# Optimization experiments

Hardware: AMD Instinct MI355X
Metric: run time of the kernel (lower is better)

The kernel has to match this reference:

```python
import jax, jax.numpy as jnp
import numpy as np

TEMPERATURE = 0.5
LAMBDA_REG = 0.1
NUM_GROUPS = 4  # number of distinct sensitive-attribute values
EPS = 1e-8      # torch cosine_similarity norm clamp


def setup_inputs() -> dict:
    key = jax.random.key(0)
    k1, k2, k3 = jax.random.split(key, 3)
    B, D = 4096, 256
    return {
        "z_i": jax.random.normal(k1, (B, D), dtype=jnp.float32),
        "z_j": jax.random.normal(k2, (B, D), dtype=jnp.float32),
        "sensitive_features": jax.random.randint(k3, (B,), 0, NUM_GROUPS, dtype=jnp.int64),
    }


def reference(z_i, z_j, sensitive_features):
    B = z_i.shape[0]
    z = jnp.concatenate([z_i, z_j], axis=0)                       # [2B, D]
    norm = jnp.maximum(jnp.linalg.norm(z, axis=1, keepdims=True), EPS)
    zn = z / norm                                                  # row-normalized
    S = zn @ zn.T                                                  # [2B, 2B] cosine sims

    # NT-Xent contrastive term
    pos = jnp.concatenate([jnp.diagonal(S, offset=B), jnp.diagonal(S, offset=-B)])  # [2B]
    mask = 1.0 - jnp.eye(2 * B, dtype=S.dtype)                     # zero out self-sims
    den = jnp.sum(mask * jnp.exp(S / TEMPERATURE), axis=1)         # [2B]
    contrastive = jnp.sum(-(pos / TEMPERATURE) + jnp.log(den)) / (2 * B)

    # Fairness penalty over groups of the FIRST B rows (indices come from sensitive_features)
    Sg = S[:B, :B]
    onehot = jax.nn.one_hot(sensitive_features, NUM_GROUPS, dtype=S.dtype)  # [B, G]
    group_sums = jnp.sum(onehot * (Sg @ onehot), axis=0)           # [G] sum_{i,j in g} S[i,j] (incl. diag, as torch)
    counts = jnp.sum(onehot, axis=0)                               # [G]
    per_group = jnp.where(counts > 1, group_sums / (counts * (counts - 1.0)), 0.0)
    num_unique = jnp.sum(counts > 0).astype(S.dtype)
    fairness = LAMBDA_REG * (jnp.sum(per_group) / num_unique)

    return contrastive + fairness
```

## Files before the change

kernel.cpp:

```cpp
#include <hip/hip_runtime.h>
#include <hip/hip_bf16.h>

typedef __attribute__((ext_vector_type(8))) short short8;
typedef __attribute__((ext_vector_type(4))) float f32x4;
typedef __attribute__((address_space(1))) const void gvoid_t;
typedef __attribute__((address_space(3))) void lvoid_t;

#define NB 4096
#define DD 256
#define TWOB 8192
#define NMACRO 1056u
#define GSUM_BLOCKS 16
#define NPART 1072u

__device__ __forceinline__ unsigned short f2bf(float f) {
  unsigned int u = __float_as_uint(f);
  u += 0x7fffu + ((u >> 16) & 1u);
  return (unsigned short)(u >> 16);
}
__device__ __forceinline__ float bf2f(unsigned short s) {
  return __uint_as_float(((unsigned int)s) << 16);
}


__global__ __launch_bounds__(256) void norm_kernel(const float* __restrict__ zi,
                                                   const float* __restrict__ zj,
                                                   float* __restrict__ wsf,
                                                   float* __restrict__ ppos,
                                                   unsigned short* __restrict__ znb) {
  __shared__ float sred[4];
  if (blockIdx.x < 32) wsf[blockIdx.x * 256 + threadIdx.x] = 0.f;
  const int lane = threadIdx.x & 63, wave = threadIdx.x >> 6;
  const int i = blockIdx.x * 4 + wave;

  float4 a = ((const float4*)(zi + (size_t)i * DD))[lane];
  float4 b = ((const float4*)(zj + (size_t)i * DD))[lane];
  float sa = a.x * a.x + a.y * a.y + a.z * a.z + a.w * a.w;
  float sb = b.x * b.x + b.y * b.y + b.z * b.z + b.w * b.w;
  float sab = a.x * b.x + a.y * b.y + a.z * b.z + a.w * b.w;
#pragma unroll
  for (int m = 32; m >= 1; m >>= 1) {
    sa += __shfl_xor(sa, m);
    sb += __shfl_xor(sb, m);
    sab += __shfl_xor(sab, m);
  }
  float ra = 1.0f / fmaxf(sqrtf(sa), 1e-8f);
  float rb = 1.0f / fmaxf(sqrtf(sb), 1e-8f);
  ushort4 oa, ob;
  oa.x = f2bf(a.x * ra); oa.y = f2bf(a.y * ra); oa.z = f2bf(a.z * ra); oa.w = f2bf(a.w * ra);
  ob.x = f2bf(b.x * rb); ob.y = f2bf(b.y * rb); ob.z = f2bf(b.z * rb); ob.w = f2bf(b.w * rb);
  ((ushort4*)(znb + (size_t)i * DD))[lane] = oa;
  ((ushort4*)(znb + (size_t)(i + NB) * DD))[lane] = ob;

  if (lane == 0) sred[wave] = sab * ra * rb;
  __syncthreads();
  if (threadIdx.x == 0)
    ppos[blockIdx.x] = sred[0] + sred[1] + sred[2] + sred[3];
}

__global__ __launch_bounds__(512, 4) void den_kernel(const int* __restrict__ sf,
                                                     float* __restrict__ wsf,
                                                     const unsigned short* __restrict__ znb,
                                                     float* __restrict__ vsum_part,
                                                     int* __restrict__ cnt_part) {
  __shared__ __align__(16) unsigned short As[3][4096];
  __shared__ __align__(16) unsigned short Bs[3][8192];

  float* den = wsf;

  const int tid = threadIdx.x;
  const int lane = tid & 63, wave = tid >> 6;
  const unsigned t_raw = blockIdx.y * 64u + blockIdx.x;
  if (t_raw >= NPART) return;
  const unsigned t_lin = (t_raw & 7u) * 134u + (t_raw >> 3);

  if (t_lin < GSUM_BLOCKS) {
    const int b = (int)t_lin;
    const int r0 = b * 256;
    float acc[4][4];
#pragma unroll
    for (int q = 0; q < 4; ++q)
#pragma unroll
      for (int e = 0; e < 4; ++e) acc[q][e] = 0.f;
    int cnt[4] = {0, 0, 0, 0};
    const int rw = r0 + wave * 32;
    for (int k = 0; k < 32; ++k) {
      int row = rw + k;
      int g = sf[row];
      ushort4 v = ((const ushort4*)(znb + (size_t)row * DD))[lane];
      float f0 = bf2f(v.x), f1 = bf2f(v.y), f2 = bf2f(v.z), f3 = bf2f(v.w);
#pragma unroll
      for (int q = 0; q < 4; ++q) {
        bool sel = (g == q);
        acc[q][0] += sel ? f0 : 0.f;
        acc[q][1] += sel ? f1 : 0.f;
        acc[q][2] += sel ? f2 : 0.f;
        acc[q][3] += sel ? f3 : 0.f;
        cnt[q] += sel ? 1 : 0;
      }
    }
    float4* lsd = (float4*)&Bs[0][0];
    int* lcnt = (int*)&As[0][0];
#pragma unroll
    for (int q = 0; q < 4; ++q) {
      float4 t;
      t.x = acc[q][0]; t.y = acc[q][1]; t.z = acc[q][2]; t.w = acc[q][3];
      lsd[(wave * 4 + q) * 64 + lane] = t;
    }
    if (lane == 0) {
#pragma unroll
      for (int q = 0; q < 4; ++q) lcnt[wave * 4 + q] = cnt[q];
    }
    __syncthreads();
    if (tid < 256) {
      int g = tid >> 6, l = tid & 63;
      float4 s = {0.f, 0.f, 0.f, 0.f};
#pragma unroll
      for (int w = 0; w < 8; ++w) {
        float4 sv = lsd[(w * 4 + g) * 64 + l];
        s.x += sv.x; s.y += sv.y; s.z += sv.z; s.w += sv.w;
      }
      ((float4*)(vsum_part + (size_t)(b * 4 + g) * 256))[l] = s;
      if (tid < 4) {
        int ci = 0;
#pragma unroll
        for (int w = 0; w < 8; ++w) ci += lcnt[w * 4 + tid];
        cnt_part[b * 4 + tid] = ci;
      }
    }
    return;
  }

  unsigned t = t_lin - GSUM_BLOCKS;
  unsigned tr = 0;
  while (t >= 32u - (tr >> 1)) { t -= 32u - (tr >> 1); ++tr; }
  unsigned c = (tr >> 1) + t;
  const size_t rowbase = (size_t)tr * 128;
  const size_t colbase = (size_t)c * 256;

  const int u = lane >> 3;
  const int cp = (lane & 7) ^ u;
  const int ri = 2 * u + (cp >> 2);
  const int kelem = (cp & 3) * 8;
  const int slot = ((((lane & 1) << 2) | (lane >> 4)) ^ ((lane >> 1) & 7));
  const int fragoff = ((lane & 15) >> 1) * 128 + slot * 16;
  const int wrow = wave & 1;
  const int wcol = wave >> 1;

  const int tch = (int)(2 * c) + (wcol >> 1);
  const float fr = (tch >= (int)tr) ? 1.f : 0.f;
  const float fc = (tch > (int)tr) ? 1.f : 0.f;

  f32x4 zero = {0.f, 0.f, 0.f, 0.f};
  f32x4 acc[4][4];
#pragma unroll
  for (int i = 0; i < 4; ++i)
#pragma unroll
    for (int j = 0; j < 4; ++j) acc[i][j] = zero;

  const unsigned short* gA = znb + (rowbase + wave * 16 + ri) * DD + kelem;
  const unsigned short* gB0 = znb + (colbase + (2 * wave) * 16 + ri) * DD + kelem;
  const unsigned short* gB1 = gB0 + 16 * DD;

  auto stage = [&](int kt, int buf) {
    __builtin_amdgcn_global_load_lds((gvoid_t*)(gA + kt * 32), (lvoid_t*)&As[buf][wave * 512], 16, 0, 0);
    __builtin_amdgcn_global_load_lds((gvoid_t*)(gB0 + kt * 32), (lvoid_t*)&Bs[buf][(2 * wave) * 512], 16, 0, 0);
    __builtin_amdgcn_global_load_lds((gvoid_t*)(gB1 + kt * 32), (lvoid_t*)&Bs[buf][(2 * wave + 1) * 512], 16, 0, 0);
  };

  stage(0, 0);
  stage(1, 1);
#pragma unroll
  for (int kt = 0; kt < 8; ++kt) {
    const int buf = kt % 3;
    if (kt < 7) asm volatile("s_waitcnt vmcnt(3)" ::: "memory");
    else        asm volatile("s_waitcnt vmcnt(0)" ::: "memory");
    __builtin_amdgcn_s_barrier();
    asm volatile("" ::: "memory");
    if (kt < 6) stage(kt + 2, (kt + 2) % 3);
    short8 af[4], bfr[4];
#pragma unroll
    for (int mi = 0; mi < 4; ++mi)
      af[mi] = *(const short8*)((const char*)&As[0][0] + buf * 8192 + (wrow * 4 + mi) * 1024 + fragoff);
#pragma unroll
    for (int ni = 0; ni < 4; ++ni)
      bfr[ni] = *(const short8*)((const char*)&Bs[0][0] + buf * 16384 + (wcol * 4 + ni) * 1024 + fragoff);
#pragma unroll
    for (int mi = 0; mi < 4; ++mi)
#pragma unroll
      for (int ni = 0; ni < 4; ++ni)
        acc[mi][ni] = __builtin_amdgcn_mfma_f32_16x16x32_bf16(af[mi], bfr[ni], acc[mi][ni], 0, 0, 0);
  }

  float rsum[4][4];
  float csum[4];
#pragma unroll
  for (int mi = 0; mi < 4; ++mi)
#pragma unroll
    for (int r = 0; r < 4; ++r) rsum[mi][r] = 0.f;
#pragma unroll
  for (int ni = 0; ni < 4; ++ni) csum[ni] = 0.f;
#pragma unroll
  for (int mi = 0; mi < 4; ++mi)
#pragma unroll
    for (int ni = 0; ni < 4; ++ni)
#pragma unroll
      for (int r = 0; r < 4; ++r) {
        float e = __expf(2.0f * acc[mi][ni][r]);
        rsum[mi][r] += e;
        csum[ni] += e;
      }
#pragma unroll
  for (int m = 1; m < 16; m <<= 1)
#pragma unroll
    for (int mi = 0; mi < 4; ++mi)
#pragma unroll
      for (int r = 0; r < 4; ++r) rsum[mi][r] += __shfl_xor(rsum[mi][r], m);
#pragma unroll
  for (int m = 16; m < 64; m <<= 1)
#pragma unroll
    for (int ni = 0; ni < 4; ++ni) csum[ni] += __shfl_xor(csum[ni], m);

  float* Lr = (float*)&As[0][0];
  float* Lc = Lr + 512;
  if ((lane & 15) == 0) {
    int h = lane >> 4;
#pragma unroll
    for (int mi = 0; mi < 4; ++mi)
#pragma unroll
      for (int r = 0; r < 4; ++r)
        Lr[wcol * 128 + wrow * 64 + mi * 16 + h * 4 + r] = rsum[mi][r] * fr;
  }
  if (lane < 16) {
#pragma unroll
    for (int ni = 0; ni < 4; ++ni)
      Lc[wrow * 256 + wcol * 64 + ni * 16 + lane] = csum[ni] * fc;
  }
  __syncthreads();
  if (tid < 256) {
    float v = Lc[tid] + Lc[256 + tid];
    if (v != 0.f) unsafeAtomicAdd(&den[colbase + tid], v);
  } else if (tid < 384) {
    int r = tid - 256;
    unsafeAtomicAdd(&den[rowbase + r], Lr[r] + Lr[128 + r] + Lr[256 + r] + Lr[384 + r]);
  }
}

__global__ __launch_bounds__(1024) void tail_kernel(const float* __restrict__ wsf,
                                                    const float* __restrict__ vsum_part,
                                                    const int* __restrict__ cnt_part,
                                                    const float* __restrict__ ppos,
                                                    float* __restrict__ out) {
  __shared__ float sred[48];
  const float* den = wsf;
  const int tid = threadIdx.x;
  const int lane = tid & 63, wave = tid >> 6;

  const float e2 = __expf(2.0f);
  float ls = 0.f;
#pragma unroll
  for (int k = 0; k < 8; ++k) ls += __logf(den[k * 1024 + tid] - e2);
#pragma unroll
  for (int m = 32; m >= 1; m >>= 1) ls += __shfl_xor(ls, m);
  if (lane == 0) sred[wave] = ls;

  float pp = ppos[tid];
#pragma unroll
  for (int m = 32; m >= 1; m >>= 1) pp += __shfl_xor(pp, m);
  if (lane == 0) sred[16 + wave] = pp;

  {
    int g = tid >> 8, col = tid & 255;
    float v = 0.f;
#pragma unroll
    for (int b = 0; b < 16; ++b) v += vsum_part[(size_t)(b * 4 + g) * 256 + col];
    float gp = v * v;
#pragma unroll
    for (int m = 32; m >= 1; m >>= 1) gp += __shfl_xor(gp, m);
    if (lane == 0) sred[32 + wave] = gp;
  }
  __syncthreads();
  if (tid == 0) {
    float lsum = 0.f, psum = 0.f;
#pragma unroll
    for (int w = 0; w < 16; ++w) { lsum += sred[w]; psum += sred[16 + w]; }
    float contrastive = (lsum - 4.0f * psum) / (float)TWOB;
    float fsum = 0.f;
    int uniq = 0;
#pragma unroll
    for (int q = 0; q < 4; ++q) {
      int ci = 0;
#pragma unroll
      for (int b = 0; b < 16; ++b) ci += cnt_part[b * 4 + q];
      float gsq = sred[32 + q * 4] + sred[33 + q * 4] + sred[34 + q * 4] + sred[35 + q * 4];
      float cf = (float)ci;
      if (ci > 0) uniq++;
      if (ci > 1) fsum += gsq / (cf * (cf - 1.0f));
    }
    out[0] = contrastive + 0.1f * (fsum / (uniq > 0 ? (float)uniq : 1.0f));
  }
}

extern "C" void kernel_launch(void* const* d_in, const int* in_sizes, int n_in,
                              void* d_out, int out_size, void* d_ws, size_t ws_size,
                              hipStream_t stream) {
  const float* zi = (const float*)d_in[0];
  const float* zj = (const float*)d_in[1];
  const int* sf = (const int*)d_in[2];
  float* out = (float*)d_out;
  char* ws = (char*)d_ws;
  float* wsf = (float*)ws;
  unsigned short* znb = (unsigned short*)(ws + 65536);
  float* vsum_part = (float*)(ws + 4259840);
  int* cnt_part = (int*)(ws + 4276224);
  float* ppos = (float*)(ws + 4276480);

  hipLaunchKernelGGL(norm_kernel, dim3(1024), dim3(256), 0, stream, zi, zj, wsf, ppos, znb);
  hipLaunchKernelGGL(den_kernel, dim3(64, 17), dim3(512), 0, stream,
                     sf, wsf, znb, vsum_part, cnt_part);
  hipLaunchKernelGGL(tail_kernel, dim3(1), dim3(1024), 0, stream,
                     wsf, vsum_part, cnt_part, ppos, out);
}
```

Baseline: 96.65 us.

## Use 256x256 symmetric tiles in den_kernel instead of 128x256

Result: slower. 102.0 us (+5.5%).

```diff
diff --git a/kernel.cpp b/kernel.cpp
--- a/kernel.cpp
+++ b/kernel.cpp
@@ -9,9 +9,9 @@
 #define NB 4096
 #define DD 256
 #define TWOB 8192
-#define NMACRO 1056u
+#define NMACRO 528u
 #define GSUM_BLOCKS 16
-#define NPART 1072u
+#define NPART 544u
 
 __device__ __forceinline__ unsigned short f2bf(float f) {
   unsigned int u = __float_as_uint(f);
@@ -58,21 +58,21 @@
     ppos[blockIdx.x] = sred[0] + sred[1] + sred[2] + sred[3];
 }
 
-__global__ __launch_bounds__(512, 4) void den_kernel(const int* __restrict__ sf,
+__global__ __launch_bounds__(512, 2) void den_kernel(const int* __restrict__ sf,
                                                      float* __restrict__ wsf,
                                                      const unsigned short* __restrict__ znb,
                                                      float* __restrict__ vsum_part,
                                                      int* __restrict__ cnt_part) {
-  __shared__ __align__(16) unsigned short As[3][4096];
+  __shared__ __align__(16) unsigned short As[3][8192];
   __shared__ __align__(16) unsigned short Bs[3][8192];
 
   float* den = wsf;
 
   const int tid = threadIdx.x;
   const int lane = tid & 63, wave = tid >> 6;
-  const unsigned t_raw = blockIdx.y * 64u + blockIdx.x;
+  const unsigned t_raw = blockIdx.y * 68u + blockIdx.x;
   if (t_raw >= NPART) return;
-  const unsigned t_lin = (t_raw & 7u) * 134u + (t_raw >> 3);
+  const unsigned t_lin = (t_raw & 7u) * 68u + (t_raw >> 3);
 
   if (t_lin < GSUM_BLOCKS) {
     const int b = (int)t_lin;
@@ -133,10 +133,11 @@
 
   unsigned t = t_lin - GSUM_BLOCKS;
   unsigned tr = 0;
-  while (t >= 32u - (tr >> 1)) { t -= 32u - (tr >> 1); ++tr; }
-  unsigned c = (tr >> 1) + t;
-  const size_t rowbase = (size_t)tr * 128;
-  const size_t colbase = (size_t)c * 256;
+  while (t >= 32u - tr) { t -= 32u - tr; ++tr; }
+  unsigned tc = tr + t;
+  const size_t rowbase = (size_t)tr * 256;
+  const size_t colbase = (size_t)tc * 256;
+  const bool offdiag = (tc > tr);
 
   const int u = lane >> 3;
   const int cp = (lane & 7) ^ u;
@@ -144,26 +145,24 @@
   const int kelem = (cp & 3) * 8;
   const int slot = ((((lane & 1) << 2) | (lane >> 4)) ^ ((lane >> 1) & 7));
   const int fragoff = ((lane & 15) >> 1) * 128 + slot * 16;
-  const int wrow = wave & 1;
-  const int wcol = wave >> 1;
-
-  const int tch = (int)(2 * c) + (wcol >> 1);
-  const float fr = (tch >= (int)tr) ? 1.f : 0.f;
-  const float fc = (tch > (int)tr) ? 1.f : 0.f;
+  const int wrow = wave >> 1;
+  const int wcol = wave & 1;
 
   f32x4 zero = {0.f, 0.f, 0.f, 0.f};
-  f32x4 acc[4][4];
+  f32x4 acc[4][8];
 #pragma unroll
   for (int i = 0; i < 4; ++i)
 #pragma unroll
-    for (int j = 0; j < 4; ++j) acc[i][j] = zero;
-
-  const unsigned short* gA = znb + (rowbase + wave * 16 + ri) * DD + kelem;
+    for (int j = 0; j < 8; ++j) acc[i][j] = zero;
+
+  const unsigned short* gA0 = znb + (rowbase + (2 * wave) * 16 + ri) * DD + kelem;
+  const unsigned short* gA1 = gA0 + 16 * DD;
   const unsigned short* gB0 = znb + (colbase + (2 * wave) * 16 + ri) * DD + kelem;
   const unsigned short* gB1 = gB0 + 16 * DD;
 
   auto stage = [&](int kt, int buf) {
-    __builtin_amdgcn_global_load_lds((gvoid_t*)(gA + kt * 32), (lvoid_t*)&As[buf][wave * 512], 16, 0, 0);
+    __builtin_amdgcn_global_load_lds((gvoid_t*)(gA0 + kt * 32), (lvoid_t*)&As[buf][(2 * wave) * 512], 16, 0, 0);
+    __builtin_amdgcn_global_load_lds((gvoid_t*)(gA1 + kt * 32), (lvoid_t*)&As[buf][(2 * wave + 1) * 512], 16, 0, 0);
     __builtin_amdgcn_global_load_lds((gvoid_t*)(gB0 + kt * 32), (lvoid_t*)&Bs[buf][(2 * wave) * 512], 16, 0, 0);
     __builtin_amdgcn_global_load_lds((gvoid_t*)(gB1 + kt * 32), (lvoid_t*)&Bs[buf][(2 * wave + 1) * 512], 16, 0, 0);
   };
@@ -173,37 +172,37 @@
 #pragma unroll
   for (int kt = 0; kt < 8; ++kt) {
     const int buf = kt % 3;
-    if (kt < 7) asm volatile("s_waitcnt vmcnt(3)" ::: "memory");
+    if (kt < 7) asm volatile("s_waitcnt vmcnt(4)" ::: "memory");
     else        asm volatile("s_waitcnt vmcnt(0)" ::: "memory");
     __builtin_amdgcn_s_barrier();
     asm volatile("" ::: "memory");
     if (kt < 6) stage(kt + 2, (kt + 2) % 3);
-    short8 af[4], bfr[4];
+    short8 af[4], bfr[8];
 #pragma unroll
     for (int mi = 0; mi < 4; ++mi)
-      af[mi] = *(const short8*)((const char*)&As[0][0] + buf * 8192 + (wrow * 4 + mi) * 1024 + fragoff);
-#pragma unroll
-    for (int ni = 0; ni < 4; ++ni)
-      bfr[ni] = *(const short8*)((const char*)&Bs[0][0] + buf * 16384 + (wcol * 4 + ni) * 1024 + fragoff);
+      af[mi] = *(const short8*)((const char*)&As[0][0] + buf * 16384 + (wrow * 4 + mi) * 1024 + fragoff);
+#pragma unroll
+    for (int ni = 0; ni < 8; ++ni)
+      bfr[ni] = *(const short8*)((const char*)&Bs[0][0] + buf * 16384 + (wcol * 8 + ni) * 1024 + fragoff);
 #pragma unroll
     for (int mi = 0; mi < 4; ++mi)
 #pragma unroll
-      for (int ni = 0; ni < 4; ++ni)
+      for (int ni = 0; ni < 8; ++ni)
         acc[mi][ni] = __builtin_amdgcn_mfma_f32_16x16x32_bf16(af[mi], bfr[ni], acc[mi][ni], 0, 0, 0);
   }
 
   float rsum[4][4];
-  float csum[4];
+  float csum[8];
 #pragma unroll
   for (int mi = 0; mi < 4; ++mi)
 #pragma unroll
     for (int r = 0; r < 4; ++r) rsum[mi][r] = 0.f;
 #pragma unroll
-  for (int ni = 0; ni < 4; ++ni) csum[ni] = 0.f;
+  for (int ni = 0; ni < 8; ++ni) csum[ni] = 0.f;
 #pragma unroll
   for (int mi = 0; mi < 4; ++mi)
 #pragma unroll
-    for (int ni = 0; ni < 4; ++ni)
+    for (int ni = 0; ni < 8; ++ni)
 #pragma unroll
       for (int r = 0; r < 4; ++r) {
         float e = __expf(2.0f * acc[mi][ni][r]);
@@ -219,7 +218,7 @@
 #pragma unroll
   for (int m = 16; m < 64; m <<= 1)
 #pragma unroll
-    for (int ni = 0; ni < 4; ++ni) csum[ni] += __shfl_xor(csum[ni], m);
+    for (int ni = 0; ni < 8; ++ni) csum[ni] += __shfl_xor(csum[ni], m);
 
   float* Lr = (float*)&As[0][0];
   float* Lc = Lr + 512;
@@ -229,20 +228,20 @@
     for (int mi = 0; mi < 4; ++mi)
 #pragma unroll
       for (int r = 0; r < 4; ++r)
-        Lr[wcol * 128 + wrow * 64 + mi * 16 + h * 4 + r] = rsum[mi][r] * fr;
+        Lr[wcol * 256 + wrow * 64 + mi * 16 + h * 4 + r] = rsum[mi][r];
   }
   if (lane < 16) {
 #pragma unroll
-    for (int ni = 0; ni < 4; ++ni)
-      Lc[wrow * 256 + wcol * 64 + ni * 16 + lane] = csum[ni] * fc;
+    for (int ni = 0; ni < 8; ++ni)
+      Lc[wrow * 256 + wcol * 128 + ni * 16 + lane] = csum[ni];
   }
   __syncthreads();
   if (tid < 256) {
-    float v = Lc[tid] + Lc[256 + tid];
-    if (v != 0.f) unsafeAtomicAdd(&den[colbase + tid], v);
-  } else if (tid < 384) {
-    int r = tid - 256;
-    unsafeAtomicAdd(&den[rowbase + r], Lr[r] + Lr[128 + r] + Lr[256 + r] + Lr[384 + r]);
+    unsafeAtomicAdd(&den[rowbase + tid], Lr[tid] + Lr[256 + tid]);
+  } else if (offdiag) {
+    int cc = tid - 256;
+    unsafeAtomicAdd(&den[colbase + cc],
+                    Lc[cc] + Lc[256 + cc] + Lc[512 + cc] + Lc[768 + cc]);
   }
 }
 
@@ -316,7 +315,7 @@
   float* ppos = (float*)(ws + 4276480);
 
   hipLaunchKernelGGL(norm_kernel, dim3(1024), dim3(256), 0, stream, zi, zj, wsf, ppos, znb);
-  hipLaunchKernelGGL(den_kernel, dim3(64, 17), dim3(512), 0, stream,
+  hipLaunchKernelGGL(den_kernel, dim3(68, 8), dim3(512), 0, stream,
                      sf, wsf, znb, vsum_part, cnt_part);
   hipLaunchKernelGGL(tail_kernel, dim3(1), dim3(1024), 0, stream,
                      wsf, vsum_part, cnt_part, ppos, out);
```

## Fuse tail reduction into den kernel and process two tiles per block

Applied to the files above, without the earlier changes.

Measured after the change: 106.5 us. 10.2% more time.

```diff
diff --git a/kernel.cpp b/kernel.cpp
--- a/kernel.cpp
+++ b/kernel.cpp
@@ -11,7 +11,7 @@
 #define TWOB 8192
 #define NMACRO 1056u
 #define GSUM_BLOCKS 16
-#define NPART 1072u
+#define NPART 544u
 
 __device__ __forceinline__ unsigned short f2bf(float f) {
   unsigned int u = __float_as_uint(f);
@@ -30,6 +30,7 @@
                                                    unsigned short* __restrict__ znb) {
   __shared__ float sred[4];
   if (blockIdx.x < 32) wsf[blockIdx.x * 256 + threadIdx.x] = 0.f;
+  if (blockIdx.x == 32 && threadIdx.x == 0) ((int*)(wsf + 8192))[0] = 0;
   const int lane = threadIdx.x & 63, wave = threadIdx.x >> 6;
   const int i = blockIdx.x * 4 + wave;
 
@@ -62,17 +63,20 @@
                                                      float* __restrict__ wsf,
                                                      const unsigned short* __restrict__ znb,
                                                      float* __restrict__ vsum_part,
-                                                     int* __restrict__ cnt_part) {
+                                                     int* __restrict__ cnt_part,
+                                                     const float* __restrict__ ppos,
+                                                     float* __restrict__ out,
+                                                     int* __restrict__ done_cnt) {
   __shared__ __align__(16) unsigned short As[3][4096];
   __shared__ __align__(16) unsigned short Bs[3][8192];
+  __shared__ __align__(16) float Escr[1024];
+  __shared__ int ilast;
 
   float* den = wsf;
-
   const int tid = threadIdx.x;
   const int lane = tid & 63, wave = tid >> 6;
-  const unsigned t_raw = blockIdx.y * 64u + blockIdx.x;
-  if (t_raw >= NPART) return;
-  const unsigned t_lin = (t_raw & 7u) * 134u + (t_raw >> 3);
+  const unsigned t_raw = blockIdx.y * 68u + blockIdx.x;
+  const unsigned t_lin = (t_raw & 7u) * 68u + (t_raw >> 3);
 
   if (t_lin < GSUM_BLOCKS) {
     const int b = (int)t_lin;
@@ -128,176 +132,206 @@
         cnt_part[b * 4 + tid] = ci;
       }
     }
-    return;
+  } else {
+    const unsigned idx = t_lin - GSUM_BLOCKS;
+    unsigned tr0, c0, tr1, c1;
+    {
+      unsigned t = 2u * idx, tr = 0;
+      while (t >= 32u - (tr >> 1)) { t -= 32u - (tr >> 1); ++tr; }
+      tr0 = tr; c0 = (tr >> 1) + t;
+      t = 2u * idx + 1u; tr = 0;
+      while (t >= 32u - (tr >> 1)) { t -= 32u - (tr >> 1); ++tr; }
+      tr1 = tr; c1 = (tr >> 1) + t;
+    }
+
+    const int u = lane >> 3;
+    const int cp = (lane & 7) ^ u;
+    const int ri = 2 * u + (cp >> 2);
+    const int kelem = (cp & 3) * 8;
+    const int slot = ((((lane & 1) << 2) | (lane >> 4)) ^ ((lane >> 1) & 7));
+    const int fragoff = ((lane & 15) >> 1) * 128 + slot * 16;
+    const int wrow = wave & 1;
+    const int wcol = wave >> 1;
+
+    f32x4 zero = {0.f, 0.f, 0.f, 0.f};
+    f32x4 acc[4][4];
+#pragma unroll
+    for (int i = 0; i < 4; ++i)
+#pragma unroll
+      for (int j = 0; j < 4; ++j) acc[i][j] = zero;
+
+    const unsigned short* gA_p0 = znb + ((size_t)tr0 * 128 + wave * 16 + ri) * DD + kelem;
+    const unsigned short* gB0_p0 = znb + ((size_t)c0 * 256 + (2 * wave) * 16 + ri) * DD + kelem;
+    const unsigned short* gB1_p0 = gB0_p0 + 16 * DD;
+    const unsigned short* gA_p1 = znb + ((size_t)tr1 * 128 + wave * 16 + ri) * DD + kelem;
+    const unsigned short* gB0_p1 = znb + ((size_t)c1 * 256 + (2 * wave) * 16 + ri) * DD + kelem;
+    const unsigned short* gB1_p1 = gB0_p1 + 16 * DD;
+
+    auto stage = [&](int s) {
+      const int buf = s % 3, kt = s & 7;
+      const unsigned short* gA = (s < 8) ? gA_p0 : gA_p1;
+      const unsigned short* gB0 = (s < 8) ? gB0_p0 : gB0_p1;
+      const unsigned short* gB1 = (s < 8) ? gB1_p0 : gB1_p1;
+      __builtin_amdgcn_global_load_lds((gvoid_t*)(gA + kt * 32), (lvoid_t*)&As[buf][wave * 512], 16, 0, 0);
+      __builtin_amdgcn_global_load_lds((gvoid_t*)(gB0 + kt * 32), (lvoid_t*)&Bs[buf][(2 * wave) * 512], 16, 0, 0);
+      __builtin_amdgcn_global_load_lds((gvoid_t*)(gB1 + kt * 32), (lvoid_t*)&Bs[buf][(2 * wave + 1) * 512], 16, 0, 0);
+    };
+
+    auto epilogue = [&](unsigned tr, unsigned c) {
+      const size_t rowbase = (size_t)tr * 128;
+      const size_t colbase = (size_t)c * 256;
+      const int tch = (int)(2 * c) + (wcol >> 1);
+      const float fr = (tch >= (int)tr) ? 1.f : 0.f;
+      const float fc = (tch > (int)tr) ? 1.f : 0.f;
+      float rsum[4][4], csum[4];
+#pragma unroll
+      for (int mi = 0; mi < 4; ++mi)
+#pragma unroll
+        for (int r = 0; r < 4; ++r) rsum[mi][r] = 0.f;
+#pragma unroll
+      for (int ni = 0; ni < 4; ++ni) csum[ni] = 0.f;
+#pragma unroll
+      for (int mi = 0; mi < 4; ++mi)
+#pragma unroll
+        for (int ni = 0; ni < 4; ++ni)
+#pragma unroll
+          for (int r = 0; r < 4; ++r) {
+            float e = __expf(2.0f * acc[mi][ni][r]);
+            rsum[mi][r] += e;
+            csum[ni] += e;
+          }
+#pragma unroll
+      for (int m = 1; m < 16; m <<= 1)
+#pragma unroll
+        for (int mi = 0; mi < 4; ++mi)
+#pragma unroll
+          for (int r = 0; r < 4; ++r) rsum[mi][r] += __shfl_xor(rsum[mi][r], m);
+#pragma unroll
+      for (int m = 16; m < 64; m <<= 1)
+#pragma unroll
+        for (int ni = 0; ni < 4; ++ni) csum[ni] += __shfl_xor(csum[ni], m);
+
+      float* Lr = &Escr[0];
+      float* Lc = &Escr[512];
+      if ((lane & 15) == 0) {
+        int h = lane >> 4;
+#pragma unroll
+        for (int mi = 0; mi < 4; ++mi)
+#pragma unroll
+          for (int r = 0; r < 4; ++r)
+            Lr[wcol * 128 + wrow * 64 + mi * 16 + h * 4 + r] = rsum[mi][r] * fr;
+      }
+      if (lane < 16) {
+#pragma unroll
+        for (int ni = 0; ni < 4; ++ni)
+          Lc[wrow * 256 + wcol * 64 + ni * 16 + lane] = csum[ni] * fc;
+      }
+      asm volatile("s_waitcnt lgkmcnt(0)" ::: "memory");
+      __builtin_amdgcn_s_barrier();
+      asm volatile("" ::: "memory");
+      if (tid < 256) {
+        float v = Lc[tid] + Lc[256 + tid];
+        if (v != 0.f) unsafeAtomicAdd(&den[colbase + tid], v);
+      } else if (tid < 384) {
+        int r = tid - 256;
+        unsafeAtomicAdd(&den[rowbase + r], Lr[r] + Lr[128 + r] + Lr[256 + r] + Lr[384 + r]);
+      }
+#pragma unroll
+      for (int i = 0; i < 4; ++i)
+#pragma unroll
+        for (int j = 0; j < 4; ++j) acc[i][j] = zero;
+    };
+
+    stage(0);
+    stage(1);
+#pragma unroll
+    for (int s = 0; s < 16; ++s) {
+      const int buf = s % 3;
+      if (s < 15) asm volatile("s_waitcnt vmcnt(4)" ::: "memory");
+      else        asm volatile("s_waitcnt vmcnt(0)" ::: "memory");
+      __builtin_amdgcn_s_barrier();
+      asm volatile("" ::: "memory");
+      if (s < 14) stage(s + 2);
+      short8 af[4], bfr[4];
+#pragma unroll
+      for (int mi = 0; mi < 4; ++mi)
+        af[mi] = *(const short8*)((const char*)&As[0][0] + buf * 8192 + (wrow * 4 + mi) * 1024 + fragoff);
+#pragma unroll
+      for (int ni = 0; ni < 4; ++ni)
+        bfr[ni] = *(const short8*)((const char*)&Bs[0][0] + buf * 16384 + (wcol * 4 + ni) * 1024 + fragoff);
+#pragma unroll
+      for (int mi = 0; mi < 4; ++mi)
+#pragma unroll
+        for (int ni = 0; ni < 4; ++ni)
+          acc[mi][ni] = __builtin_amdgcn_mfma_f32_16x16x32_bf16(af[mi], bfr[ni], acc[mi][ni], 0, 0, 0);
+      if (s == 7) epilogue(tr0, c0);
+    }
+    epilogue(tr1, c1);
   }
 
-  unsigned t = t_lin - GSUM_BLOCKS;
-  unsigned tr = 0;
-  while (t >= 32u - (tr >> 1)) { t -= 32u - (tr >> 1); ++tr; }
-  unsigned c = (tr >> 1) + t;
-  const size_t rowbase = (size_t)tr * 128;
-  const size_t colbase = (size_t)c * 256;
-
-  const int u = lane >> 3;
-  const int cp = (lane & 7) ^ u;
-  const int ri = 2 * u + (cp >> 2);
-  const int kelem = (cp & 3) * 8;
-  const int slot = ((((lane & 1) << 2) | (lane >> 4)) ^ ((lane >> 1) & 7));
-  const int fragoff = ((lane & 15) >> 1) * 128 + slot * 16;
-  const int wrow = wave & 1;
-  const int wcol = wave >> 1;
-
-  const int tch = (int)(2 * c) + (wcol >> 1);
-  const float fr = (tch >= (int)tr) ? 1.f : 0.f;
-  const float fc = (tch > (int)tr) ? 1.f : 0.f;
-
-  f32x4 zero = {0.f, 0.f, 0.f, 0.f};
-  f32x4 acc[4][4];
-#pragma unroll
-  for (int i = 0; i < 4; ++i)
-#pragma unroll
-    for (int j = 0; j < 4; ++j) acc[i][j] = zero;
-
-  const unsigned short* gA = znb + (rowbase + wave * 16 + ri) * DD + kelem;
-  const unsigned short* gB0 = znb + (colbase + (2 * wave) * 16 + ri) * DD + kelem;
-  const unsigned short* gB1 = gB0 + 16 * DD;
-
-  auto stage = [&](int kt, int buf) {
-    __builtin_amdgcn_global_load_lds((gvoid_t*)(gA + kt * 32), (lvoid_t*)&As[buf][wave * 512], 16, 0, 0);
-    __builtin_amdgcn_global_load_lds((gvoid_t*)(gB0 + kt * 32), (lvoid_t*)&Bs[buf][(2 * wave) * 512], 16, 0, 0);
-    __builtin_amdgcn_global_load_lds((gvoid_t*)(gB1 + kt * 32), (lvoid_t*)&Bs[buf][(2 * wave + 1) * 512], 16, 0, 0);
-  };
-
-  stage(0, 0);
-  stage(1, 1);
-#pragma unroll
-  for (int kt = 0; kt < 8; ++kt) {
-    const int buf = kt % 3;
-    if (kt < 7) asm volatile("s_waitcnt vmcnt(3)" ::: "memory");
-    else        asm volatile("s_waitcnt vmcnt(0)" ::: "memory");
-    __builtin_amdgcn_s_barrier();
-    asm volatile("" ::: "memory");
-    if (kt < 6) stage(kt + 2, (kt + 2) % 3);
-    short8 af[4], bfr[4];
-#pragma unroll
-    for (int mi = 0; mi < 4; ++mi)
-      af[mi] = *(const short8*)((const char*)&As[0][0] + buf * 8192 + (wrow * 4 + mi) * 1024 + fragoff);
-#pragma unroll
-    for (int ni = 0; ni < 4; ++ni)
-      bfr[ni] = *(const short8*)((const char*)&Bs[0][0] + buf * 16384 + (wcol * 4 + ni) * 1024 + fragoff);
-#pragma unroll
-    for (int mi = 0; mi < 4; ++mi)
-#pragma unroll
-      for (int ni = 0; ni < 4; ++ni)
-        acc[mi][ni] = __builtin_amdgcn_mfma_f32_16x16x32_bf16(af[mi], bfr[ni], acc[mi][ni], 0, 0, 0);
-  }
-
-  float rsum[4][4];
-  float csum[4];
-#pragma unroll
-  for (int mi = 0; mi < 4; ++mi)
-#pragma unroll
-    for (int r = 0; r < 4; ++r) rsum[mi][r] = 0.f;
-#pragma unroll
-  for (int ni = 0; ni < 4; ++ni) csum[ni] = 0.f;
-#pragma unroll
-  for (int mi = 0; mi < 4; ++mi)
-#pragma unroll
-    for (int ni = 0; ni < 4; ++ni)
-#pragma unroll
-      for (int r = 0; r < 4; ++r) {
-        float e = __expf(2.0f * acc[mi][ni][r]);
-        rsum[mi][r] += e;
-        csum[ni] += e;
-      }
-#pragma unroll
-  for (int m = 1; m < 16; m <<= 1)
-#pragma unroll
-    for (int mi = 0; mi < 4; ++mi)
-#pragma unroll
-      for (int r = 0; r < 4; ++r) rsum[mi][r] += __shfl_xor(rsum[mi][r], m);
-#pragma unroll
-  for (int m = 16; m < 64; m <<= 1)
-#pragma unroll
-    for (int ni = 0; ni < 4; ++ni) csum[ni] += __shfl_xor(csum[ni], m);
-
-  float* Lr = (float*)&As[0][0];
-  float* Lc = Lr + 512;
-  if ((lane & 15) == 0) {
-    int h = lane >> 4;
-#pragma unroll
-    for (int mi = 0; mi < 4; ++mi)
-#pragma unroll
-      for (int r = 0; r < 4; ++r)
-        Lr[wcol * 128 + wrow * 64 + mi * 16 + h * 4 + r] = rsum[mi][r] * fr;
-  }
-  if (lane < 16) {
-#pragma unroll
-    for (int ni = 0; ni < 4; ++ni)
-      Lc[wrow * 256 + wcol * 64 + ni * 16 + lane] = csum[ni] * fc;
+  __syncthreads();
+  if (tid == 0) {
+    if (t_lin < GSUM_BLOCKS) __threadfence();
+    int prev = __hip_atomic_fetch_add(done_cnt, 1, __ATOMIC_RELAXED, __HIP_MEMORY_SCOPE_AGENT);
+    ilast = (prev == (int)NPART - 1) ? 1 : 0;
   }
   __syncthreads();
-  if (tid < 256) {
-    float v = Lc[tid] + Lc[256 + tid];
-    if (v != 0.f) unsafeAtomicAdd(&den[colbase + tid], v);
-  } else if (tid < 384) {
-    int r = tid - 256;
-    unsafeAtomicAdd(&den[rowbase + r], Lr[r] + Lr[128 + r] + Lr[256 + r] + Lr[384 + r]);
-  }
-}
-
-__global__ __launch_bounds__(1024) void tail_kernel(const float* __restrict__ wsf,
-                                                    const float* __restrict__ vsum_part,
-                                                    const int* __restrict__ cnt_part,
-                                                    const float* __restrict__ ppos,
-                                                    float* __restrict__ out) {
-  __shared__ float sred[48];
-  const float* den = wsf;
-  const int tid = threadIdx.x;
-  const int lane = tid & 63, wave = tid >> 6;
-
-  const float e2 = __expf(2.0f);
-  float ls = 0.f;
-#pragma unroll
-  for (int k = 0; k < 8; ++k) ls += __logf(den[k * 1024 + tid] - e2);
-#pragma unroll
-  for (int m = 32; m >= 1; m >>= 1) ls += __shfl_xor(ls, m);
-  if (lane == 0) sred[wave] = ls;
-
-  float pp = ppos[tid];
-#pragma unroll
-  for (int m = 32; m >= 1; m >>= 1) pp += __shfl_xor(pp, m);
-  if (lane == 0) sred[16 + wave] = pp;
+  if (ilast == 0) return;
 
   {
-    int g = tid >> 8, col = tid & 255;
-    float v = 0.f;
-#pragma unroll
-    for (int b = 0; b < 16; ++b) v += vsum_part[(size_t)(b * 4 + g) * 256 + col];
-    float gp = v * v;
-#pragma unroll
-    for (int m = 32; m >= 1; m >>= 1) gp += __shfl_xor(gp, m);
-    if (lane == 0) sred[32 + wave] = gp;
-  }
-  __syncthreads();
-  if (tid == 0) {
-    float lsum = 0.f, psum = 0.f;
-#pragma unroll
-    for (int w = 0; w < 16; ++w) { lsum += sred[w]; psum += sred[16 + w]; }
-    float contrastive = (lsum - 4.0f * psum) / (float)TWOB;
-    float fsum = 0.f;
-    int uniq = 0;
-#pragma unroll
-    for (int q = 0; q < 4; ++q) {
-      int ci = 0;
-#pragma unroll
-      for (int b = 0; b < 16; ++b) ci += cnt_part[b * 4 + q];
-      float gsq = sred[32 + q * 4] + sred[33 + q * 4] + sred[34 + q * 4] + sred[35 + q * 4];
-      float cf = (float)ci;
-      if (ci > 0) uniq++;
-      if (ci > 1) fsum += gsq / (cf * (cf - 1.0f));
-    }
-    out[0] = contrastive + 0.1f * (fsum / (uniq > 0 ? (float)uniq : 1.0f));
+    float* sred = &Escr[0];
+    const float e2 = __expf(2.0f);
+    float ls = 0.f;
+#pragma unroll
+    for (int k = 0; k < 16; ++k) {
+      float d = __hip_atomic_load(&wsf[k * 512 + tid], __ATOMIC_RELAXED, __HIP_MEMORY_SCOPE_AGENT);
+      ls += __logf(d - e2);
+    }
+#pragma unroll
+    for (int m = 32; m >= 1; m >>= 1) ls += __shfl_xor(ls, m);
+    if (lane == 0) sred[wave] = ls;
+
+    float pp = ppos[tid] + ppos[512 + tid];
+#pragma unroll
+    for (int m = 32; m >= 1; m >>= 1) pp += __shfl_xor(pp, m);
+    if (lane == 0) sred[8 + wave] = pp;
+
+    {
+      int g = tid >> 7, col2 = tid & 127;
+      float v1 = 0.f, v2 = 0.f;
+#pragma unroll
+      for (int b = 0; b < 16; ++b) {
+        v1 += __hip_atomic_load(&vsum_part[(size_t)(b * 4 + g) * 256 + col2],
+                                __ATOMIC_RELAXED, __HIP_MEMORY_SCOPE_AGENT);
+        v2 += __hip_atomic_load(&vsum_part[(size_t)(b * 4 + g) * 256 + col2 + 128],
+                                __ATOMIC_RELAXED, __HIP_MEMORY_SCOPE_AGENT);
+      }
+      float gp = v1 * v1 + v2 * v2;
+#pragma unroll
+      for (int m = 32; m >= 1; m >>= 1) gp += __shfl_xor(gp, m);
+      if (lane == 0) sred[16 + wave] = gp;
+    }
+    __syncthreads();
+    if (tid == 0) {
+      float lsum = 0.f, psum = 0.f;
+#pragma unroll
+      for (int w = 0; w < 8; ++w) { lsum += sred[w]; psum += sred[8 + w]; }
+      float contrastive = (lsum - 4.0f * psum) / (float)TWOB;
+      float fsum = 0.f;
+      int uniq = 0;
+#pragma unroll
+      for (int q = 0; q < 4; ++q) {
+        int ci = 0;
+#pragma unroll
+        for (int b = 0; b < 16; ++b)
+          ci += __hip_atomic_load(&cnt_part[b * 4 + q], __ATOMIC_RELAXED, __HIP_MEMORY_SCOPE_AGENT);
+        float gsq = sred[16 + 2 * q] + sred[17 + 2 * q];
+        float cf = (float)ci;
+        if (ci > 0) uniq++;
+        if (ci > 1) fsum += gsq / (cf * (cf - 1.0f));
+      }
+      out[0] = contrastive + 0.1f * (fsum / (uniq > 0 ? (float)uniq : 1.0f));
+    }
   }
 }
 
@@ -310,14 +344,13 @@
   float* out = (float*)d_out;
   char* ws = (char*)d_ws;
   float* wsf = (float*)ws;
+  int* done_cnt = (int*)(ws + 32768);
   unsigned short* znb = (unsigned short*)(ws + 65536);
   float* vsum_part = (float*)(ws + 4259840);
   int* cnt_part = (int*)(ws + 4276224);
   float* ppos = (float*)(ws + 4276480);
 
   hipLaunchKernelGGL(norm_kernel, dim3(1024), dim3(256), 0, stream, zi, zj, wsf, ppos, znb);
-  hipLaunchKernelGGL(den_kernel, dim3(64, 17), dim3(512), 0, stream,
-                     sf, wsf, znb, vsum_part, cnt_part);
-  hipLaunchKernelGGL(tail_kernel, dim3(1), dim3(1024), 0, stream,
-                     wsf, vsum_part, cnt_part, ppos, out);
-}
+  hipLaunchKernelGGL(den_kernel, dim3(68, 8), dim3(512), 0, stream,
+                     sf, wsf, znb, vsum_part, cnt_part, ppos, out, done_cnt);
+}
```

## Reorder triangular tile schedule into 8x8 super-blocks via precomputed lookup table

Applied to the files above, without the earlier changes.

Measured after the change: 99.70 us. 3.2% more time.

```diff
diff --git a/kernel.cpp b/kernel.cpp
--- a/kernel.cpp
+++ b/kernel.cpp
@@ -12,6 +12,7 @@
 #define NMACRO 1056u
 #define GSUM_BLOCKS 16
 #define NPART 1072u
+#define TBL_OFF 36864
 
 __device__ __forceinline__ unsigned short f2bf(float f) {
   unsigned int u = __float_as_uint(f);
@@ -62,7 +63,8 @@
                                                      float* __restrict__ wsf,
                                                      const unsigned short* __restrict__ znb,
                                                      float* __restrict__ vsum_part,
-                                                     int* __restrict__ cnt_part) {
+                                                     int* __restrict__ cnt_part,
+                                                     const unsigned short* __restrict__ tbl) {
   __shared__ __align__(16) unsigned short As[3][4096];
   __shared__ __align__(16) unsigned short Bs[3][8192];
 
@@ -131,10 +133,9 @@
     return;
   }
 
-  unsigned t = t_lin - GSUM_BLOCKS;
-  unsigned tr = 0;
-  while (t >= 32u - (tr >> 1)) { t -= 32u - (tr >> 1); ++tr; }
-  unsigned c = (tr >> 1) + t;
+  const unsigned tv = tbl[t_lin - GSUM_BLOCKS];
+  const unsigned tr = tv >> 8;
+  const unsigned c = tv & 255u;
   const size_t rowbase = (size_t)tr * 128;
   const size_t colbase = (size_t)c * 256;
 
@@ -310,14 +311,32 @@
   float* out = (float*)d_out;
   char* ws = (char*)d_ws;
   float* wsf = (float*)ws;
+  unsigned short* tblw = (unsigned short*)(ws + TBL_OFF);
   unsigned short* znb = (unsigned short*)(ws + 65536);
   float* vsum_part = (float*)(ws + 4259840);
   int* cnt_part = (int*)(ws + 4276224);
   float* ppos = (float*)(ws + 4276480);
 
+  static unsigned short tile_tbl[NMACRO];
+  static bool tbl_init = false;
+  if (!tbl_init) {
+    int idx = 0;
+    for (int trb = 0; trb < 8; ++trb)
+      for (int cb = 0; cb < 4; ++cb)
+        for (int i = 0; i < 8; ++i) {
+          int tr = trb * 8 + i;
+          for (int j = 0; j < 8; ++j) {
+            int c = cb * 8 + j;
+            if (c >= tr / 2) tile_tbl[idx++] = (unsigned short)((tr << 8) | c);
+          }
+        }
+    tbl_init = true;
+  }
+  hipMemcpyAsync(tblw, tile_tbl, sizeof(tile_tbl), hipMemcpyHostToDevice, stream);
+
   hipLaunchKernelGGL(norm_kernel, dim3(1024), dim3(256), 0, stream, zi, zj, wsf, ppos, znb);
   hipLaunchKernelGGL(den_kernel, dim3(64, 17), dim3(512), 0, stream,
-                     sf, wsf, znb, vsum_part, cnt_part);
+                     sf, wsf, znb, vsum_part, cnt_part, tblw);
   hipLaunchKernelGGL(tail_kernel, dim3(1), dim3(1024), 0, stream,
                      wsf, vsum_part, cnt_part, ppos, out);
 }
```
